# Performance work log

Measured on AMD Instinct MI355X. Metric: run time of the kernel, lower is better.

Reference implementation:

```python
import jax, jax.numpy as jnp
import numpy as np

BN_EPS = 1e-5
TN_EPS = 1e-4


def binarize(x):
    # Clipped straight-through binarization (Courbariaux BNN / Brevitas 1-bit):
    # forward = sign(x) in {-1,+1}, backward = hardtanh STE.
    xc = jnp.clip(x, -1.0, 1.0)
    return xc + jax.lax.stop_gradient(jnp.where(x >= 0, 1.0, -1.0).astype(x.dtype) - xc)


def setup_inputs() -> dict:
    key = jax.random.key(0)
    ks = jax.random.split(key, 20)
    B, D, H, C = 16384, 1024, 1024, 10
    inp = {"x": jax.random.uniform(ks[0], (B, D), dtype=jnp.float32)}
    dims = [(H, D), (H, H), (H, H), (C, H)]
    for i, (o, n) in enumerate(dims):
        inp[f"W{i+1}"] = jax.random.uniform(ks[1 + i], (o, n), minval=-1.0, maxval=1.0, dtype=jnp.float32)
    # BatchNorm1d params (eval mode, running stats) for the 3 hidden layers
    for i in range(3):
        k0, k1, k2, k3 = jax.random.split(ks[5 + i], 4)
        inp[f"g{i+1}"] = 1.0 + 0.1 * jax.random.normal(k0, (H,), dtype=jnp.float32)
        inp[f"b{i+1}"] = 0.1 * jax.random.normal(k1, (H,), dtype=jnp.float32)
        inp[f"m{i+1}"] = 0.1 * jax.random.normal(k2, (H,), dtype=jnp.float32)
        inp[f"v{i+1}"] = 0.5 + jax.random.uniform(k3, (H,), dtype=jnp.float32)
    # TensorNorm (scalar norm on the logits)
    inp["tn_w"] = jnp.ones((), dtype=jnp.float32)
    inp["tn_b"] = jnp.zeros((), dtype=jnp.float32)
    inp["tn_m"] = jnp.zeros((), dtype=jnp.float32)
    inp["tn_v"] = jnp.ones((), dtype=jnp.float32)
    return inp


def reference(x, W1, W2, W3, W4,
              g1, b1, m1, v1,
              g2, b2, m2, v2,
              g3, b3, m3, v3,
              tn_w, tn_b, tn_m, tn_v):
    h = binarize(2.0 * x.reshape(x.shape[0], -1) - 1.0)
    # Dropout is identity in eval mode.
    bn = [(g1, b1, m1, v1), (g2, b2, m2, v2), (g3, b3, m3, v3)]
    for W, (g, b, m, v) in zip((W1, W2, W3), bn):
        h = h @ binarize(W).T                      # [B,H] fake-quant linear, no bias
        h = (h - m) * (g * jax.lax.rsqrt(v + BN_EPS)) + b  # BatchNorm1d eval
        h = binarize(h)                            # 1-bit activation quant
    h = h @ binarize(W4).T                         # [B,10]
    # TensorNorm: scalar affine normalization over the whole tensor
    return (h - tn_m) * jax.lax.rsqrt(tn_v + TN_EPS) * tn_w + tn_b
```

## Files before the change

kernel.cpp:

```cpp
#include <hip/hip_runtime.h>
#include <stdint.h>

typedef int  v4i  __attribute__((ext_vector_type(4)));
typedef int  v16i __attribute__((ext_vector_type(16)));
typedef unsigned int uint32;

#define BATCH 16384
#define FEAT  1024

#define OFF_ACTA 0u
#define OFF_ACTB 16777216u
#define OFF_WA1  33554432u
#define OFF_WA2  34603008u
#define OFF_WA3  35651584u
#define OFF_WA4  36700160u
#define OFF_TH   36732928u

__global__ void __launch_bounds__(256) prep_kernel(
    const float* __restrict__ x,
    const float* __restrict__ W1, const float* __restrict__ W2,
    const float* __restrict__ W3, const float* __restrict__ W4,
    const float* __restrict__ g1, const float* __restrict__ b1,
    const float* __restrict__ m1, const float* __restrict__ v1,
    const float* __restrict__ g2, const float* __restrict__ b2,
    const float* __restrict__ m2, const float* __restrict__ v2,
    const float* __restrict__ g3, const float* __restrict__ b3,
    const float* __restrict__ m3, const float* __restrict__ v3,
    char* __restrict__ actA, char* __restrict__ wa1, char* __restrict__ wa2,
    char* __restrict__ wa3, char* __restrict__ wa4, int* __restrict__ TH)
{
    int b = blockIdx.x;
    if (b == 609) {
        for (int gid = threadIdx.x; gid < 3072; gid += 256) {
            int l = gid >> 10, j = gid & 1023;
            const float *g, *bb, *m, *v;
            if (l == 0)      { g = g1; bb = b1; m = m1; v = v1; }
            else if (l == 1) { g = g2; bb = b2; m = m2; v = v2; }
            else             { g = g3; bb = b3; m = m3; v = v3; }
            double gd = (double)g[j], bd = (double)bb[j], md = (double)m[j], vd = (double)v[j];
            double s = gd / sqrt(vd + 1e-5);
            int t2;
            if (s > 0.0)      t2 = (int)ceil(md - bd / s);
            else if (s < 0.0) t2 = -(int)floor(md - bd / s);
            else              t2 = (bd >= 0.0) ? -2000000 : 2000000;
            TH[gid] = t2;
        }
        return;
    }

    const float* src; char* dst; float thr; int nrows; int dblk;
    const float* gp = nullptr;
    if (b < 512)      { src = x  + (size_t)b * 32768;            dst = actA; dblk = b;      thr = 0.5f; nrows = 32; }
    else if (b < 544) { int mb = b - 512; src = W1 + (size_t)mb * 32768; dst = wa1; dblk = mb; thr = 0.0f; nrows = 32; gp = g1; }
    else if (b < 576) { int mb = b - 544; src = W2 + (size_t)mb * 32768; dst = wa2; dblk = mb; thr = 0.0f; nrows = 32; gp = g2; }
    else if (b < 608) { int mb = b - 576; src = W3 + (size_t)mb * 32768; dst = wa3; dblk = mb; thr = 0.0f; nrows = 32; gp = g3; }
    else              { src = W4; dst = wa4; dblk = 0; thr = 0.0f; nrows = 10; }

    __shared__ unsigned char T[32][1040];
#pragma unroll
    for (int u = 0; u < 8; ++u) {
        int unit = threadIdx.x + u * 256;
        int row  = unit >> 6;
        int c16  = (unit & 63) << 4;
        uint32 wb0 = 0, wb1 = 0, wb2 = 0, wb3 = 0;
        if (row < nrows) {
            bool flipb = gp && (gp[dblk * 32 + row] < 0.0f);
            const float* p = src + (size_t)row * 1024 + c16;
            float4 f0 = *(const float4*)(p + 0);
            float4 f1 = *(const float4*)(p + 4);
            float4 f2 = *(const float4*)(p + 8);
            float4 f3 = *(const float4*)(p + 12);
#define BY(f) ((((f) >= thr) != flipb) ? 0x01u : 0xFFu)
            wb0 = BY(f0.x) | (BY(f0.y)<<8) | (BY(f0.z)<<16) | (BY(f0.w)<<24);
            wb1 = BY(f1.x) | (BY(f1.y)<<8) | (BY(f1.z)<<16) | (BY(f1.w)<<24);
            wb2 = BY(f2.x) | (BY(f2.y)<<8) | (BY(f2.z)<<16) | (BY(f2.w)<<24);
            wb3 = BY(f3.x) | (BY(f3.y)<<8) | (BY(f3.z)<<16) | (BY(f3.w)<<24);
#undef BY
        }
        *(uint4*)&T[row][c16] = make_uint4(wb0, wb1, wb2, wb3);
    }
    __syncthreads();

    int lane = threadIdx.x & 63;
    int wv   = threadIdx.x >> 6;
    int row  = lane & 31;
    int hb   = (lane >> 5) * 4;
#pragma unroll
    for (int u = 0; u < 8; ++u) {
        int kk = wv * 8 + u;
        const unsigned char* tr = &T[row][kk * 32 + hb];
        uint32 w0 = *(const uint32*)(tr + 0);
        uint32 w1 = *(const uint32*)(tr + 8);
        uint32 w2 = *(const uint32*)(tr + 16);
        uint32 w3 = *(const uint32*)(tr + 24);
        *(uint4*)(dst + (((size_t)dblk * 32 + kk) * 64 + lane) * 16) = make_uint4(w0, w1, w2, w3);
    }
}

__device__ __forceinline__ void gload16(const v4i* gsrc, v4i* ldst) {
    __builtin_amdgcn_global_load_lds(
        (const __attribute__((address_space(1))) void*)gsrc,
        (__attribute__((address_space(3))) void*)ldst, 16, 0, 0);
}

__global__ void __launch_bounds__(256, 2) gemm_i8_kernel(
    const v4i* __restrict__ Af, const v4i* __restrict__ Bin,
    const int* __restrict__ th, v4i* __restrict__ Bout)
{
    __shared__ v4i Bs[2][2048];
    __shared__ int Tsh[128];
    const int tid  = threadIdx.x;
    const int lane = tid & 63;
    const int wv   = tid >> 6;
    int bid = blockIdx.x;
    int xcd = bid & 7;
    int i   = bid >> 3;
    int s   = xcd + ((i >> 3) << 3);
    int m   = i & 7;
    int mt  = m * 4 + wv;
    int nb0 = s * 8;

#pragma unroll
    for (int j = 0; j < 8; ++j)
        gload16(Bin + (size_t)nb0 * 2048 + j * 256 + wv * 64 + lane,
                &Bs[0][j * 256 + wv * 64]);
    if (tid < 128) Tsh[tid] = th[m * 128 + tid];

    v4i a[32];
    {
        const v4i* Ap = Af + (size_t)mt * 2048;
#pragma unroll
        for (int kk = 0; kk < 32; ++kk) a[kk] = Ap[kk * 64 + lane];
    }
    asm volatile("s_waitcnt vmcnt(0) lgkmcnt(0)" ::: "memory");
    __builtin_amdgcn_s_barrier();

    const int hi4 = (lane >> 5) * 4;
    int tq[16];
#pragma unroll
    for (int q = 0; q < 16; ++q) tq[q] = -Tsh[wv * 32 + (q & 3) + 8 * (q >> 2) + hi4];

    int buf = 0;
#pragma unroll 1
    for (int it = 0; it < 8; ++it) {
        const v4i* Bb = &Bs[buf][0];
        v4i* Bn = &Bs[buf ^ 1][0];
        const v4i* gnext = Bin + (size_t)(nb0 + it + 1) * 2048;

        v16i acc0, acc1;
#pragma unroll
        for (int q = 0; q < 16; ++q) { acc0[q] = tq[q]; acc1[q] = 0; }

        v4i c0 = Bb[0 * 64 + lane], c1 = Bb[1 * 64 + lane];
        v4i c2 = Bb[16 * 64 + lane], c3 = Bb[17 * 64 + lane];

#pragma unroll
        for (int p = 0; p < 8; ++p) {
            v4i n0, n1, n2, n3;
            if (p < 7) {
                n0 = Bb[(2 * p + 2) * 64 + lane];
                n1 = Bb[(2 * p + 3) * 64 + lane];
                n2 = Bb[(18 + 2 * p) * 64 + lane];
                n3 = Bb[(19 + 2 * p) * 64 + lane];
            }
            if (p < 4 && it < 7) {
                int j = 2 * p;
                gload16(gnext + j * 256 + wv * 64 + lane,       Bn + j * 256 + wv * 64);
                gload16(gnext + (j + 1) * 256 + wv * 64 + lane, Bn + (j + 1) * 256 + wv * 64);
            }
            __builtin_amdgcn_s_setprio(1);
            acc0 = __builtin_amdgcn_mfma_i32_32x32x32_i8(a[2 * p],      c0, acc0, 0, 0, 0);
            acc1 = __builtin_amdgcn_mfma_i32_32x32x32_i8(a[16 + 2 * p], c2, acc1, 0, 0, 0);
            acc0 = __builtin_amdgcn_mfma_i32_32x32x32_i8(a[2 * p + 1],  c1, acc0, 0, 0, 0);
            acc1 = __builtin_amdgcn_mfma_i32_32x32x32_i8(a[17 + 2 * p], c3, acc1, 0, 0, 0);
            __builtin_amdgcn_s_setprio(0);
            c0 = n0; c1 = n1; c2 = n2; c3 = n3;
        }

        uint32 wds0 = 0, wds1 = 0, wds2 = 0, wds3 = 0;
#pragma unroll
        for (int bq = 0; bq < 4; ++bq) {
            { int h = acc0[bq]      + acc1[bq];      wds0 |= (((uint32)((h >> 31) | 1)) & 0xFFu) << (8 * bq); }
            { int h = acc0[4 + bq]  + acc1[4 + bq];  wds1 |= (((uint32)((h >> 31) | 1)) & 0xFFu) << (8 * bq); }
            { int h = acc0[8 + bq]  + acc1[8 + bq];  wds2 |= (((uint32)((h >> 31) | 1)) & 0xFFu) << (8 * bq); }
            { int h = acc0[12 + bq] + acc1[12 + bq]; wds3 |= (((uint32)((h >> 31) | 1)) & 0xFFu) << (8 * bq); }
        }
        v4i ov; ov[0] = (int)wds0; ov[1] = (int)wds1; ov[2] = (int)wds2; ov[3] = (int)wds3;
        Bout[((size_t)(nb0 + it) * 32 + mt) * 64 + lane] = ov;

        if (it < 7) {
            asm volatile("s_waitcnt vmcnt(1)" ::: "memory");
            __builtin_amdgcn_s_barrier();
            buf ^= 1;
        }
    }
}

__global__ void __launch_bounds__(128) final_kernel(
    const v4i* __restrict__ Af4, const v4i* __restrict__ B3,
    const float* __restrict__ tw, const float* __restrict__ tb,
    const float* __restrict__ tm, const float* __restrict__ tv,
    float* __restrict__ out)
{
    int lane = threadIdx.x & 63;
    int nb   = blockIdx.x * 2 + (threadIdx.x >> 6);
    const v4i* Bf = B3 + (size_t)nb * 2048;
    v16i acc;
#pragma unroll
    for (int z = 0; z < 16; ++z) acc[z] = 0;
#pragma unroll
    for (int kk = 0; kk < 32; ++kk) {
        v4i av = Af4[kk * 64 + lane];
        v4i bv = Bf[kk * 64 + lane];
        acc = __builtin_amdgcn_mfma_i32_32x32x32_i8(av, bv, acc, 0, 0, 0);
    }
    double sc  = (double)tw[0] / sqrt((double)tv[0] + 1e-4);
    double off = (double)tb[0] - (double)tm[0] * sc;
    int colg = nb * 32 + (lane & 31);
    int hi   = lane >> 5;
#pragma unroll
    for (int q = 0; q < 8; ++q) {
        int rr = (q & 3) + 8 * (q >> 2) + 4 * hi;
        if (rr < 10)
            out[(size_t)colg * 10 + rr] = (float)((double)acc[q] * sc + off);
    }
}

extern "C" void kernel_launch(void* const* d_in, const int* in_sizes, int n_in,
                              void* d_out, int out_size, void* d_ws, size_t ws_size,
                              hipStream_t stream) {
    const float* x  = (const float*)d_in[0];
    const float* W1 = (const float*)d_in[1];
    const float* W2 = (const float*)d_in[2];
    const float* W3 = (const float*)d_in[3];
    const float* W4 = (const float*)d_in[4];
    const float* g1 = (const float*)d_in[5];
    const float* b1 = (const float*)d_in[6];
    const float* m1 = (const float*)d_in[7];
    const float* v1 = (const float*)d_in[8];
    const float* g2 = (const float*)d_in[9];
    const float* b2 = (const float*)d_in[10];
    const float* m2 = (const float*)d_in[11];
    const float* v2 = (const float*)d_in[12];
    const float* g3 = (const float*)d_in[13];
    const float* b3 = (const float*)d_in[14];
    const float* m3 = (const float*)d_in[15];
    const float* v3 = (const float*)d_in[16];
    const float* tw = (const float*)d_in[17];
    const float* tb = (const float*)d_in[18];
    const float* tm = (const float*)d_in[19];
    const float* tv = (const float*)d_in[20];

    char* ws = (char*)d_ws;
    char* actA = ws + OFF_ACTA;
    char* actB = ws + OFF_ACTB;
    char* wa1  = ws + OFF_WA1;
    char* wa2  = ws + OFF_WA2;
    char* wa3  = ws + OFF_WA3;
    char* wa4  = ws + OFF_WA4;
    int*  TH   = (int*)(ws + OFF_TH);

    prep_kernel<<<610, 256, 0, stream>>>(x, W1, W2, W3, W4,
                                         g1, b1, m1, v1, g2, b2, m2, v2,
                                         g3, b3, m3, v3,
                                         actA, wa1, wa2, wa3, wa4, TH);

    gemm_i8_kernel<<<512, 256, 0, stream>>>((const v4i*)wa1, (const v4i*)actA, TH,        (v4i*)actB);
    gemm_i8_kernel<<<512, 256, 0, stream>>>((const v4i*)wa2, (const v4i*)actB, TH + 1024, (v4i*)actA);
    gemm_i8_kernel<<<512, 256, 0, stream>>>((const v4i*)wa3, (const v4i*)actA, TH + 2048, (v4i*)actB);

    final_kernel<<<256, 128, 0, stream>>>((const v4i*)wa4, (const v4i*)actB,
                                          tw, tb, tm, tv, (float*)d_out);
}
```

Baseline: 200.8 us.

## Fuse prep, three GEMM layers and final into one persistent kernel with grid barriers

Merges the five kernel launches (prep, three binary int8 GEMM layers, final logits) into a single persistent kernel of 512 blocks that separates stages with a software grid-wide atomic barrier. The prep transpose buffer now reuses the GEMM shared-memory array. This targets per-launch overhead and inter-kernel gaps. In exchange it adds barrier spin cost, and it relies on all 512 blocks being co-resident. The barrier's spin timeout also risks silently breaking correctness if residency is not guaranteed. A memset of the barrier counters is added before launch.

```diff
diff --git a/kernel.cpp b/kernel.cpp
--- a/kernel.cpp
+++ b/kernel.cpp
@@ -7,6 +7,7 @@
 
 #define BATCH 16384
 #define FEAT  1024
+#define GRID  512
 
 #define OFF_ACTA 0u
 #define OFF_ACTB 16777216u
@@ -15,48 +16,77 @@
 #define OFF_WA3  35651584u
 #define OFF_WA4  36700160u
 #define OFF_TH   36732928u
-
-__global__ void __launch_bounds__(256) prep_kernel(
-    const float* __restrict__ x,
-    const float* __restrict__ W1, const float* __restrict__ W2,
-    const float* __restrict__ W3, const float* __restrict__ W4,
-    const float* __restrict__ g1, const float* __restrict__ b1,
-    const float* __restrict__ m1, const float* __restrict__ v1,
-    const float* __restrict__ g2, const float* __restrict__ b2,
-    const float* __restrict__ m2, const float* __restrict__ v2,
-    const float* __restrict__ g3, const float* __restrict__ b3,
-    const float* __restrict__ m3, const float* __restrict__ v3,
-    char* __restrict__ actA, char* __restrict__ wa1, char* __restrict__ wa2,
-    char* __restrict__ wa3, char* __restrict__ wa4, int* __restrict__ TH)
+#define OFF_BAR  36745216u
+
+struct KArgs {
+    const float *x, *W1, *W2, *W3, *W4;
+    const float *g1, *b1, *m1, *v1;
+    const float *g2, *b2, *m2, *v2;
+    const float *g3, *b3, *m3, *v3;
+    const float *tw, *tb, *tm, *tv;
+    char *actA, *actB, *wa1, *wa2, *wa3, *wa4;
+    int *TH;
+    int *bar;
+    float *out;
+};
+
+__device__ __forceinline__ void grid_barrier(int* bar)
 {
-    int b = blockIdx.x;
+    __syncthreads();
+    if (threadIdx.x == 0) {
+        __threadfence();
+        int g = __hip_atomic_load(&bar[1], __ATOMIC_RELAXED, __HIP_MEMORY_SCOPE_AGENT);
+        int n = __hip_atomic_fetch_add(&bar[0], 1, __ATOMIC_ACQ_REL, __HIP_MEMORY_SCOPE_AGENT);
+        if (n == GRID - 1) {
+            __hip_atomic_store(&bar[0], 0,     __ATOMIC_RELAXED, __HIP_MEMORY_SCOPE_AGENT);
+            __hip_atomic_store(&bar[1], g + 1, __ATOMIC_RELEASE, __HIP_MEMORY_SCOPE_AGENT);
+        } else {
+            long spin = 0;
+            while (__hip_atomic_load(&bar[1], __ATOMIC_ACQUIRE, __HIP_MEMORY_SCOPE_AGENT) == g) {
+                __builtin_amdgcn_s_sleep(8);
+                if (++spin > (1L << 20)) break;
+            }
+        }
+        __threadfence();
+    }
+    __syncthreads();
+}
+
+__device__ __forceinline__ void gload16(const v4i* gsrc, v4i* ldst) {
+    __builtin_amdgcn_global_load_lds(
+        (const __attribute__((address_space(1))) void*)gsrc,
+        (__attribute__((address_space(3))) void*)ldst, 16, 0, 0);
+}
+
+__device__ __forceinline__ void prep_unit(int b, const KArgs& P,
+                                          unsigned char (*T)[1040])
+{
     if (b == 609) {
         for (int gid = threadIdx.x; gid < 3072; gid += 256) {
             int l = gid >> 10, j = gid & 1023;
             const float *g, *bb, *m, *v;
-            if (l == 0)      { g = g1; bb = b1; m = m1; v = v1; }
-            else if (l == 1) { g = g2; bb = b2; m = m2; v = v2; }
-            else             { g = g3; bb = b3; m = m3; v = v3; }
+            if (l == 0)      { g = P.g1; bb = P.b1; m = P.m1; v = P.v1; }
+            else if (l == 1) { g = P.g2; bb = P.b2; m = P.m2; v = P.v2; }
+            else             { g = P.g3; bb = P.b3; m = P.m3; v = P.v3; }
             double gd = (double)g[j], bd = (double)bb[j], md = (double)m[j], vd = (double)v[j];
             double s = gd / sqrt(vd + 1e-5);
             int t2;
             if (s > 0.0)      t2 = (int)ceil(md - bd / s);
             else if (s < 0.0) t2 = -(int)floor(md - bd / s);
             else              t2 = (bd >= 0.0) ? -2000000 : 2000000;
-            TH[gid] = t2;
+            P.TH[gid] = t2;
         }
         return;
     }
 
     const float* src; char* dst; float thr; int nrows; int dblk;
     const float* gp = nullptr;
-    if (b < 512)      { src = x  + (size_t)b * 32768;            dst = actA; dblk = b;      thr = 0.5f; nrows = 32; }
-    else if (b < 544) { int mb = b - 512; src = W1 + (size_t)mb * 32768; dst = wa1; dblk = mb; thr = 0.0f; nrows = 32; gp = g1; }
-    else if (b < 576) { int mb = b - 544; src = W2 + (size_t)mb * 32768; dst = wa2; dblk = mb; thr = 0.0f; nrows = 32; gp = g2; }
-    else if (b < 608) { int mb = b - 576; src = W3 + (size_t)mb * 32768; dst = wa3; dblk = mb; thr = 0.0f; nrows = 32; gp = g3; }
-    else              { src = W4; dst = wa4; dblk = 0; thr = 0.0f; nrows = 10; }
-
-    __shared__ unsigned char T[32][1040];
+    if (b < 512)      { src = P.x  + (size_t)b * 32768;            dst = P.actA; dblk = b;      thr = 0.5f; nrows = 32; }
+    else if (b < 544) { int mb = b - 512; src = P.W1 + (size_t)mb * 32768; dst = P.wa1; dblk = mb; thr = 0.0f; nrows = 32; gp = P.g1; }
+    else if (b < 576) { int mb = b - 544; src = P.W2 + (size_t)mb * 32768; dst = P.wa2; dblk = mb; thr = 0.0f; nrows = 32; gp = P.g2; }
+    else if (b < 608) { int mb = b - 576; src = P.W3 + (size_t)mb * 32768; dst = P.wa3; dblk = mb; thr = 0.0f; nrows = 32; gp = P.g3; }
+    else              { src = P.W4; dst = P.wa4; dblk = 0; thr = 0.0f; nrows = 10; }
+
 #pragma unroll
     for (int u = 0; u < 8; ++u) {
         int unit = threadIdx.x + u * 256;
@@ -95,20 +125,13 @@
         uint32 w3 = *(const uint32*)(tr + 24);
         *(uint4*)(dst + (((size_t)dblk * 32 + kk) * 64 + lane) * 16) = make_uint4(w0, w1, w2, w3);
     }
-}
-
-__device__ __forceinline__ void gload16(const v4i* gsrc, v4i* ldst) {
-    __builtin_amdgcn_global_load_lds(
-        (const __attribute__((address_space(1))) void*)gsrc,
-        (__attribute__((address_space(3))) void*)ldst, 16, 0, 0);
-}
-
-__global__ void __launch_bounds__(256, 2) gemm_i8_kernel(
-    const v4i* __restrict__ Af, const v4i* __restrict__ Bin,
-    const int* __restrict__ th, v4i* __restrict__ Bout)
+    __syncthreads();
+}
+
+__device__ __forceinline__ void layer_gemm(const v4i* __restrict__ Af,
+    const v4i* __restrict__ Bin, const int* __restrict__ th,
+    v4i* __restrict__ Bout, v4i (*Bs)[2048], int* Tsh)
 {
-    __shared__ v4i Bs[2][2048];
-    __shared__ int Tsh[128];
     const int tid  = threadIdx.x;
     const int lane = tid & 63;
     const int wv   = tid >> 6;
@@ -196,79 +219,83 @@
     }
 }
 
-__global__ void __launch_bounds__(128) final_kernel(
-    const v4i* __restrict__ Af4, const v4i* __restrict__ B3,
-    const float* __restrict__ tw, const float* __restrict__ tb,
-    const float* __restrict__ tm, const float* __restrict__ tv,
-    float* __restrict__ out)
+__global__ void __launch_bounds__(256, 2) fused_kernel(KArgs P)
 {
-    int lane = threadIdx.x & 63;
-    int nb   = blockIdx.x * 2 + (threadIdx.x >> 6);
-    const v4i* Bf = B3 + (size_t)nb * 2048;
-    v16i acc;
-#pragma unroll
-    for (int z = 0; z < 16; ++z) acc[z] = 0;
-#pragma unroll
-    for (int kk = 0; kk < 32; ++kk) {
-        v4i av = Af4[kk * 64 + lane];
-        v4i bv = Bf[kk * 64 + lane];
-        acc = __builtin_amdgcn_mfma_i32_32x32x32_i8(av, bv, acc, 0, 0, 0);
-    }
-    double sc  = (double)tw[0] / sqrt((double)tv[0] + 1e-4);
-    double off = (double)tb[0] - (double)tm[0] * sc;
-    int colg = nb * 32 + (lane & 31);
-    int hi   = lane >> 5;
-#pragma unroll
-    for (int q = 0; q < 8; ++q) {
-        int rr = (q & 3) + 8 * (q >> 2) + 4 * hi;
-        if (rr < 10)
-            out[(size_t)colg * 10 + rr] = (float)((double)acc[q] * sc + off);
+    __shared__ v4i Bs[2][2048];
+    __shared__ int Tsh[128];
+
+    {
+        unsigned char (*T)[1040] = (unsigned char (*)[1040])(&Bs[0][0]);
+        for (int b = blockIdx.x; b < 610; b += GRID)
+            prep_unit(b, P, T);
+    }
+    grid_barrier(P.bar);
+
+    layer_gemm((const v4i*)P.wa1, (const v4i*)P.actA, P.TH,        (v4i*)P.actB, Bs, Tsh);
+    grid_barrier(P.bar);
+    layer_gemm((const v4i*)P.wa2, (const v4i*)P.actB, P.TH + 1024, (v4i*)P.actA, Bs, Tsh);
+    grid_barrier(P.bar);
+    layer_gemm((const v4i*)P.wa3, (const v4i*)P.actA, P.TH + 2048, (v4i*)P.actB, Bs, Tsh);
+    grid_barrier(P.bar);
+
+    {
+        const int lane = threadIdx.x & 63;
+        const int wv   = threadIdx.x >> 6;
+        if (wv == 0) {
+            int nb = blockIdx.x;
+            const v4i* Bf  = (const v4i*)P.actB + (size_t)nb * 2048;
+            const v4i* Af4 = (const v4i*)P.wa4;
+            v16i acc;
+#pragma unroll
+            for (int z = 0; z < 16; ++z) acc[z] = 0;
+#pragma unroll
+            for (int kk = 0; kk < 32; ++kk) {
+                v4i av = Af4[kk * 64 + lane];
+                v4i bv = Bf[kk * 64 + lane];
+                acc = __builtin_amdgcn_mfma_i32_32x32x32_i8(av, bv, acc, 0, 0, 0);
+            }
+            double sc  = (double)P.tw[0] / sqrt((double)P.tv[0] + 1e-4);
+            double off = (double)P.tb[0] - (double)P.tm[0] * sc;
+            int colg = nb * 32 + (lane & 31);
+            int hi   = lane >> 5;
+#pragma unroll
+            for (int q = 0; q < 8; ++q) {
+                int rr = (q & 3) + 8 * (q >> 2) + 4 * hi;
+                if (rr < 10)
+                    P.out[(size_t)colg * 10 + rr] = (float)((double)acc[q] * sc + off);
+            }
+        }
     }
 }
 
 extern "C" void kernel_launch(void* const* d_in, const int* in_sizes, int n_in,
                               void* d_out, int out_size, void* d_ws, size_t ws_size,
                               hipStream_t stream) {
-    const float* x  = (const float*)d_in[0];
-    const float* W1 = (const float*)d_in[1];
-    const float* W2 = (const float*)d_in[2];
-    const float* W3 = (const float*)d_in[3];
-    const float* W4 = (const float*)d_in[4];
-    const float* g1 = (const float*)d_in[5];
-    const float* b1 = (const float*)d_in[6];
-    const float* m1 = (const float*)d_in[7];
-    const float* v1 = (const float*)d_in[8];
-    const float* g2 = (const float*)d_in[9];
-    const float* b2 = (const float*)d_in[10];
-    const float* m2 = (const float*)d_in[11];
-    const float* v2 = (const float*)d_in[12];
-    const float* g3 = (const float*)d_in[13];
-    const float* b3 = (const float*)d_in[14];
-    const float* m3 = (const float*)d_in[15];
-    const float* v3 = (const float*)d_in[16];
-    const float* tw = (const float*)d_in[17];
-    const float* tb = (const float*)d_in[18];
-    const float* tm = (const float*)d_in[19];
-    const float* tv = (const float*)d_in[20];
-
     char* ws = (char*)d_ws;
-    char* actA = ws + OFF_ACTA;
-    char* actB = ws + OFF_ACTB;
-    char* wa1  = ws + OFF_WA1;
-    char* wa2  = ws + OFF_WA2;
-    char* wa3  = ws + OFF_WA3;
-    char* wa4  = ws + OFF_WA4;
-    int*  TH   = (int*)(ws + OFF_TH);
-
-    prep_kernel<<<610, 256, 0, stream>>>(x, W1, W2, W3, W4,
-                                         g1, b1, m1, v1, g2, b2, m2, v2,
-                                         g3, b3, m3, v3,
-                                         actA, wa1, wa2, wa3, wa4, TH);
-
-    gemm_i8_kernel<<<512, 256, 0, stream>>>((const v4i*)wa1, (const v4i*)actA, TH,        (v4i*)actB);
-    gemm_i8_kernel<<<512, 256, 0, stream>>>((const v4i*)wa2, (const v4i*)actB, TH + 1024, (v4i*)actA);
-    gemm_i8_kernel<<<512, 256, 0, stream>>>((const v4i*)wa3, (const v4i*)actA, TH + 2048, (v4i*)actB);
-
-    final_kernel<<<256, 128, 0, stream>>>((const v4i*)wa4, (const v4i*)actB,
-                                          tw, tb, tm, tv, (float*)d_out);
-}
+    KArgs P;
+    P.x  = (const float*)d_in[0];
+    P.W1 = (const float*)d_in[1];
+    P.W2 = (const float*)d_in[2];
+    P.W3 = (const float*)d_in[3];
+    P.W4 = (const float*)d_in[4];
+    P.g1 = (const float*)d_in[5];  P.b1 = (const float*)d_in[6];
+    P.m1 = (const float*)d_in[7];  P.v1 = (const float*)d_in[8];
+    P.g2 = (const float*)d_in[9];  P.b2 = (const float*)d_in[10];
+    P.m2 = (const float*)d_in[11]; P.v2 = (const float*)d_in[12];
+    P.g3 = (const float*)d_in[13]; P.b3 = (const float*)d_in[14];
+    P.m3 = (const float*)d_in[15]; P.v3 = (const float*)d_in[16];
+    P.tw = (const float*)d_in[17]; P.tb = (const float*)d_in[18];
+    P.tm = (const float*)d_in[19]; P.tv = (const float*)d_in[20];
+    P.actA = ws + OFF_ACTA;
+    P.actB = ws + OFF_ACTB;
+    P.wa1  = ws + OFF_WA1;
+    P.wa2  = ws + OFF_WA2;
+    P.wa3  = ws + OFF_WA3;
+    P.wa4  = ws + OFF_WA4;
+    P.TH   = (int*)(ws + OFF_TH);
+    P.bar  = (int*)(ws + OFF_BAR);
+    P.out  = (float*)d_out;
+
+    hipMemsetAsync(ws + OFF_BAR, 0, 64, stream);
+    fused_kernel<<<dim3(GRID), dim3(256), 0, stream>>>(P);
+}
```

New measurement: 580.5 us. 189% more time.
